# Optimization experiments

Measured on AMD Instinct MI355X. Metric: run time of the kernel, lower is better.

The kernel has to match this reference:

```python
import jax, jax.numpy as jnp
import numpy as np

N_NODES = 100000
N_EDGES = 1600000
IN_DIM, H1, H2, OUT_DIM = 128, 64, 32, 16


def setup_inputs() -> dict:
    key = jax.random.key(0)
    ks = jax.random.split(key, 9)
    x = jax.random.normal(ks[0], (N_NODES, IN_DIM), dtype=jnp.float32)
    edge_index = jax.random.randint(ks[1], (2, N_EDGES), 0, N_NODES, dtype=jnp.int64)
    # nn.Linear-style params (out_feats, in_feats) + bias
    def lin(k, o, i):
        bound = 1.0 / np.sqrt(i)
        kw, kb = jax.random.split(k)
        W = jax.random.uniform(kw, (o, i), jnp.float32, -bound, bound)
        b = jax.random.uniform(kb, (o,), jnp.float32, -bound, bound)
        return W, b
    W1, b1 = lin(ks[2], H1, IN_DIM)
    W2, b2 = lin(ks[3], H2, H1)
    Wf, bf = lin(ks[4], OUT_DIM, H2)
    return {"x": x, "edge_index": edge_index, "W1": W1, "b1": b1,
            "W2": W2, "b2": b2, "Wf": Wf, "bf": bf}


def reference(x, edge_index, W1, b1, W2, b2, Wf, bf):
    # Original: adj = to_dense_adj(edge_index); graph built from adj.T; DGL
    # copy_src+sum then gives new_h[src] = sum over dst of h[dst], i.e. A @ h
    # with A[src, dst]. No activation between layers (unused in forward),
    # dropout inactive at inference.
    N = x.shape[0]
    src, dst = edge_index[0], edge_index[1]

    def aggregate(h):  # sum of out-neighbor features: [N, d]
        return jax.ops.segment_sum(h[dst], src, num_segments=N)

    h = aggregate(x) @ W1.T + b1          # [N, 64]
    h = aggregate(h) @ W2.T + b2          # [N, 32]
    pooled = jnp.max(h, axis=0)           # [32] global max pool over nodes
    return pooled @ Wf.T + bf             # [16]
```

## Files before the change

kernel.cpp:

```cpp
#include <hip/hip_runtime.h>

#define N_NODES 100000
#define N_EDGES 1600000
#define IN_DIM 128
#define H1_DIM 64
#define H2_DIM 32
#define OUT_DIM 16

#define NPB 128
#define KB 782
#define OFFW (KB + 1)
#define NCH 256
#define CH_E (N_EDGES / NCH)
#define CAP2 3072
#define NBIN1 64
#define NBIN2 (NCH - NBIN1)
#define NGB 782

typedef __attribute__((ext_vector_type(8))) short short8;
typedef __attribute__((ext_vector_type(4))) float f32x4;

__device__ inline unsigned short f2b(float v) {
    unsigned u = __float_as_uint(v);
    u += 0x7FFF + ((u >> 16) & 1);
    return (unsigned short)(u >> 16);
}
__device__ inline short f2bs(float v) { return (short)f2b(v); }
__device__ inline unsigned f32_to_key(float v) {
    unsigned u = __float_as_uint(v);
    return (v >= 0.f) ? (u | 0x80000000u) : ~u;
}
__device__ __forceinline__ void acc8(float* a, uint4 v) {
    a[0] += __uint_as_float(v.x << 16);
    a[1] += __uint_as_float(v.x & 0xFFFF0000u);
    a[2] += __uint_as_float(v.y << 16);
    a[3] += __uint_as_float(v.y & 0xFFFF0000u);
    a[4] += __uint_as_float(v.z << 16);
    a[5] += __uint_as_float(v.z & 0xFFFF0000u);
    a[6] += __uint_as_float(v.w << 16);
    a[7] += __uint_as_float(v.w & 0xFFFF0000u);
}

__device__ __forceinline__ void bin_chunk(const int* __restrict__ src,
                                          const int* __restrict__ dst,
                                          unsigned* __restrict__ off,
                                          unsigned* __restrict__ grec, int c) {
    __shared__ int hist[1024];
    __shared__ int part[512];
    __shared__ int cur[1024];
    int t = threadIdx.x;
    int e0 = c * CH_E;
    hist[t] = 0; hist[t + 512] = 0;
    __syncthreads();
    for (int e = t; e < CH_E; e += 512) atomicAdd(&hist[src[e0 + e] >> 7], 1);
    __syncthreads();
    int h0 = hist[2 * t], h1 = hist[2 * t + 1];
    int tot = h0 + h1;
    part[t] = tot;
    __syncthreads();
    for (int o = 1; o < 512; o <<= 1) {
        int a = (t >= o) ? part[t - o] : 0;
        __syncthreads();
        part[t] += a;
        __syncthreads();
    }
    int gb = part[t] - tot;
    int o0 = gb, o1 = gb + h0;
    int b2i = 2 * t;
    cur[b2i] = o0; cur[b2i + 1] = o1;
    if (b2i + 0 < KB) off[(size_t)c * OFFW + b2i + 0] = o0;
    if (b2i + 1 < KB) off[(size_t)c * OFFW + b2i + 1] = o1;
    if (t == 0) off[(size_t)c * OFFW + KB] = CH_E;
    __syncthreads();
    for (int e = t; e < CH_E; e += 512) {
        int s = src[e0 + e];
        int d = dst[e0 + e];
        int p = atomicAdd(&cur[s >> 7], 1);
        grec[(size_t)e0 + p] = ((unsigned)(s & 127) << 17) | (unsigned)d;
    }
}

__global__ __launch_bounds__(512) void k1_kernel(const int* __restrict__ src,
                                                 const int* __restrict__ dst,
                                                 unsigned* __restrict__ off,
                                                 unsigned* __restrict__ grec,
                                                 const float* __restrict__ W1,
                                                 const float* __restrict__ b1,
                                                 const float* __restrict__ W2,
                                                 unsigned short* __restrict__ Wcb,
                                                 float* __restrict__ cvb) {
    if (blockIdx.x < NBIN1) {
        bin_chunk(src, dst, off, grec, blockIdx.x);
        return;
    }
    int t = threadIdx.x;
    for (int idx = t; idx < H2_DIM * IN_DIM; idx += 512) {
        int j = idx >> 7, f = idx & 127;
        float acc = 0.f;
        for (int k = 0; k < H1_DIM; ++k)
            acc += W2[j * H1_DIM + k] * W1[k * IN_DIM + f];
        Wcb[idx] = f2b(acc);
    }
    if (t < H2_DIM) {
        float s = 0.f;
        for (int k = 0; k < H1_DIM; ++k) s += W2[t * H1_DIM + k] * b1[k];
        cvb[t] = s;
    }
}

__global__ __launch_bounds__(512) void k2_kernel(const int* __restrict__ src,
                                                 const int* __restrict__ dst,
                                                 unsigned* __restrict__ off,
                                                 unsigned* __restrict__ grec,
                                                 const float* __restrict__ x,
                                                 const unsigned short* __restrict__ Wcb,
                                                 unsigned short* __restrict__ yb) {
    if (blockIdx.x < NBIN2) {
        bin_chunk(src, dst, off, grec, NBIN1 + blockIdx.x);
        return;
    }
    int gb = blockIdx.x - NBIN2;
    int t = threadIdx.x;
    int w = t >> 6, l = t & 63;
    int row = l & 15, kg = l >> 4;
    int base = gb * 128 + w * 16;
    int node = base + row;
    int nclamp = (node < N_NODES) ? node : (N_NODES - 1);
    const float* xp = x + (size_t)nclamp * IN_DIM + kg * 8;
    const unsigned short* b0p = Wcb + (size_t)row * IN_DIM + kg * 8;
    const unsigned short* b1p = Wcb + (size_t)(16 + row) * IN_DIM + kg * 8;
    f32x4 acc0 = {0.f, 0.f, 0.f, 0.f}, acc1 = {0.f, 0.f, 0.f, 0.f};
#pragma unroll
    for (int kk = 0; kk < 4; ++kk) {
        float4 xa = *(const float4*)(xp + kk * 32);
        float4 xb = *(const float4*)(xp + kk * 32 + 4);
        short8 a;
        a[0] = f2bs(xa.x); a[1] = f2bs(xa.y); a[2] = f2bs(xa.z); a[3] = f2bs(xa.w);
        a[4] = f2bs(xb.x); a[5] = f2bs(xb.y); a[6] = f2bs(xb.z); a[7] = f2bs(xb.w);
        short8 b0 = *(const short8*)(b0p + kk * 32);
        short8 b1 = *(const short8*)(b1p + kk * 32);
        acc0 = __builtin_amdgcn_mfma_f32_16x16x32_bf16(a, b0, acc0, 0, 0, 0);
        acc1 = __builtin_amdgcn_mfma_f32_16x16x32_bf16(a, b1, acc1, 0, 0, 0);
    }
#pragma unroll
    for (int r = 0; r < 4; ++r) {
        int n2 = base + kg * 4 + r;
        if (n2 < N_NODES) {
            yb[(size_t)n2 * H2_DIM + row]      = f2b(acc0[r]);
            yb[(size_t)n2 * H2_DIM + 16 + row] = f2b(acc1[r]);
        }
    }
}

__global__ __launch_bounds__(512) void agg1_kernel(const unsigned short* __restrict__ in,
                                                   const unsigned* __restrict__ off,
                                                   const unsigned* __restrict__ grec,
                                                   unsigned* __restrict__ grec2,
                                                   unsigned* __restrict__ noff,
                                                   unsigned short* __restrict__ z1b) {
    __shared__ int pos[NCH + 1], sst[NCH];
    __shared__ int shist[NPB], scur2[NPB];
    __shared__ int sscan[NPB + 1];
    __shared__ unsigned rbuf[CAP2];
    __shared__ unsigned sbuf[CAP2];
    __shared__ int s_cnt;
    int t = threadIdx.x;
    int b = blockIdx.x;
    int gid = t >> 4;
    int L = t & 15;
    int chunk = L & 3, subset = L >> 2;

    int mylen = 0;
    if (t < NCH) {
        unsigned o0 = off[(size_t)t * OFFW + b];
        unsigned o1 = off[(size_t)t * OFFW + b + 1];
        sst[t] = (int)o0;
        mylen = (int)(o1 - o0);
        pos[t] = mylen;
    }
    __syncthreads();
    for (int o = 1; o < NCH; o <<= 1) {
        int a = (t < NCH && t >= o) ? pos[t - o] : 0;
        __syncthreads();
        if (t < NCH) pos[t] += a;
        __syncthreads();
    }
    if (t < NCH) pos[t] -= mylen;
    if (t == NCH - 1) {
        pos[NCH] = pos[t] + mylen;
        s_cnt = min(pos[t] + mylen, CAP2);
    }
    __syncthreads();
    int cnt = s_cnt;
    for (int i = t; i < cnt; i += 512) {
        int lo = 0, hi = NCH;
#pragma unroll
        for (int s = 0; s < 8; ++s) {
            int mid = (lo + hi) >> 1;
            if (pos[mid] <= i) lo = mid; else hi = mid;
        }
        rbuf[i] = grec[(size_t)lo * CH_E + sst[lo] + (i - pos[lo])];
    }
    if (t < NPB) shist[t] = 0;
    __syncthreads();
    for (int i = t; i < cnt; i += 512) atomicAdd(&shist[rbuf[i] >> 17], 1);
    __syncthreads();
    if (t < NPB) scur2[t] = shist[t];
    __syncthreads();
    for (int o = 1; o < NPB; o <<= 1) {
        int a = (t < NPB && t >= o) ? scur2[t - o] : 0;
        __syncthreads();
        if (t < NPB) scur2[t] += a;
        __syncthreads();
    }
    if (t < NPB) sscan[t] = scur2[t] - shist[t];
    if (t == NPB - 1) sscan[NPB] = scur2[t];
    __syncthreads();
    if (t < NPB) scur2[t] = sscan[t];
    __syncthreads();
    for (int i = t; i < cnt; i += 512) {
        unsigned r = rbuf[i];
        int p = atomicAdd(&scur2[r >> 17], 1);
        if (p < CAP2) sbuf[p] = r;
    }
    __syncthreads();
    for (int i = t; i < cnt; i += 512) grec2[(size_t)b * CAP2 + i] = sbuf[i];
    if (t < NPB + 1) noff[(size_t)b * (NPB + 1) + t] = (unsigned)sscan[t];
    __syncthreads();

    for (int sl = gid; sl < NPB; sl += 32) {
        int r0 = sscan[sl], r1 = sscan[sl + 1];
        float a[8] = {0.f, 0.f, 0.f, 0.f, 0.f, 0.f, 0.f, 0.f};
        float aa[8] = {0.f, 0.f, 0.f, 0.f, 0.f, 0.f, 0.f, 0.f};
        for (int e = r0; e < r1; e += 8) {
            int eA = e + subset, eB = e + 4 + subset;
            if (eA < r1) {
                unsigned rc = sbuf[eA];
                uint4 v = *(const uint4*)(in + (size_t)(rc & 0x1FFFFu) * H2_DIM + chunk * 8);
                acc8(a, v);
            }
            if (eB < r1) {
                unsigned rc = sbuf[eB];
                uint4 v = *(const uint4*)(in + (size_t)(rc & 0x1FFFFu) * H2_DIM + chunk * 8);
                acc8(aa, v);
            }
        }
#pragma unroll
        for (int j = 0; j < 8; ++j) {
            float s = a[j] + aa[j];
            s += __shfl_xor(s, 4);
            s += __shfl_xor(s, 8);
            a[j] = s;
        }
        int node = b * NPB + sl;
        if (node < N_NODES && subset == 0) {
            uint4 o;
            o.x = (unsigned)f2b(a[0]) | ((unsigned)f2b(a[1]) << 16);
            o.y = (unsigned)f2b(a[2]) | ((unsigned)f2b(a[3]) << 16);
            o.z = (unsigned)f2b(a[4]) | ((unsigned)f2b(a[5]) << 16);
            o.w = (unsigned)f2b(a[6]) | ((unsigned)f2b(a[7]) << 16);
            *(uint4*)(z1b + (size_t)node * H2_DIM + chunk * 8) = o;
        }
    }
}

__global__ __launch_bounds__(1024) void agg2_kernel(const unsigned short* __restrict__ in,
                                                    const unsigned* __restrict__ grec2,
                                                    const unsigned* __restrict__ noff,
                                                    const float* __restrict__ cvb,
                                                    const float* __restrict__ b2,
                                                    unsigned* __restrict__ pk) {
    __shared__ float smq[64][4][8];
    int t = threadIdx.x;
    int b = blockIdx.x;
    int gid = t >> 4;
    int L = t & 15;
    int chunk = L & 3, subset = L >> 2;

    const unsigned* rp = grec2 + (size_t)b * CAP2;
    const unsigned* np = noff + (size_t)b * (NPB + 1);

    float m[8];
#pragma unroll
    for (int j = 0; j < 8; ++j) m[j] = -3.402823466e+38f;

    for (int sl = gid; sl < NPB; sl += 64) {
        int r0 = (int)np[sl], r1 = (int)np[sl + 1];
        float a[8] = {0.f, 0.f, 0.f, 0.f, 0.f, 0.f, 0.f, 0.f};
        float aa[8] = {0.f, 0.f, 0.f, 0.f, 0.f, 0.f, 0.f, 0.f};
        for (int e = r0; e < r1; e += 8) {
            int eA = e + subset, eB = e + 4 + subset;
            if (eA < r1) {
                unsigned rc = rp[eA];
                uint4 v = *(const uint4*)(in + (size_t)(rc & 0x1FFFFu) * H2_DIM + chunk * 8);
                acc8(a, v);
            }
            if (eB < r1) {
                unsigned rc = rp[eB];
                uint4 v = *(const uint4*)(in + (size_t)(rc & 0x1FFFFu) * H2_DIM + chunk * 8);
                acc8(aa, v);
            }
        }
#pragma unroll
        for (int j = 0; j < 8; ++j) {
            float s = a[j] + aa[j];
            s += __shfl_xor(s, 4);
            s += __shfl_xor(s, 8);
            a[j] = s;
        }
        int node = b * NPB + sl;
        if (node < N_NODES) {
            float dg = (float)(r1 - r0);
#pragma unroll
            for (int j = 0; j < 8; ++j)
                m[j] = fmaxf(m[j], a[j] + dg * cvb[chunk * 8 + j] + b2[chunk * 8 + j]);
        }
    }
    if (subset == 0) {
#pragma unroll
        for (int j = 0; j < 8; ++j) smq[gid][chunk][j] = m[j];
    }
    __syncthreads();
    if (t < 32) {
        int c = t >> 3, j = t & 7;
        float mm = smq[0][c][j];
#pragma unroll
        for (int k = 1; k < 64; ++k) mm = fmaxf(mm, smq[k][c][j]);
        atomicMax(&pk[t], f32_to_key(mm));
    }
}

__global__ void final_kernel(const unsigned* __restrict__ pk,
                             const float* __restrict__ Wf,
                             const float* __restrict__ bfv,
                             float* __restrict__ out) {
    __shared__ float pooled[H2_DIM];
    int t = threadIdx.x;
    if (t < H2_DIM) {
        unsigned k = pk[t];
        unsigned u = (k & 0x80000000u) ? (k & 0x7FFFFFFFu) : ~k;
        pooled[t] = __uint_as_float(u);
    }
    __syncthreads();
    if (t < OUT_DIM) {
        float acc = bfv[t];
        for (int j = 0; j < H2_DIM; ++j)
            acc += Wf[t * H2_DIM + j] * pooled[j];
        out[t] = acc;
    }
}

extern "C" void kernel_launch(void* const* d_in, const int* in_sizes, int n_in,
                              void* d_out, int out_size, void* d_ws, size_t ws_size,
                              hipStream_t stream) {
    const float* x  = (const float*)d_in[0];
    const int*   ei = (const int*)d_in[1];
    const float* W1 = (const float*)d_in[2];
    const float* b1 = (const float*)d_in[3];
    const float* W2 = (const float*)d_in[4];
    const float* b2 = (const float*)d_in[5];
    const float* Wf = (const float*)d_in[6];
    const float* bf = (const float*)d_in[7];
    float* out = (float*)d_out;

    const int* src = ei;
    const int* dst = ei + N_EDGES;

    unsigned short* yb  = (unsigned short*)d_ws;
    unsigned short* z1b = yb + (size_t)N_NODES * H2_DIM;
    unsigned short* Wcb = z1b + (size_t)N_NODES * H2_DIM;
    float* cvb      = (float*)(Wcb + H2_DIM * IN_DIM);
    unsigned* pk    = (unsigned*)(cvb + H2_DIM);
    unsigned* off   = pk + H2_DIM;
    unsigned* grec  = off + (size_t)NCH * OFFW;
    unsigned* grec2 = grec + N_EDGES;
    unsigned* noff  = grec2 + (size_t)KB * CAP2;

    hipMemsetAsync(pk, 0, H2_DIM * sizeof(unsigned), stream);

    k1_kernel<<<NBIN1 + 1, 512, 0, stream>>>(src, dst, off, grec, W1, b1, W2, Wcb, cvb);
    k2_kernel<<<NBIN2 + NGB, 512, 0, stream>>>(src, dst, off, grec, x, Wcb, yb);

    agg1_kernel<<<KB, 512, 0, stream>>>(yb, off, grec, grec2, noff, z1b);
    agg2_kernel<<<KB, 1024, 0, stream>>>(z1b, grec2, noff, cvb, b2, pk);

    final_kernel<<<1, 64, 0, stream>>>(pk, Wf, bf, out);
}
```

Measured before the change: 111.4 us.

## Use wavefront shuffle scans, transpose offset table, fold pool-init memset into k1

Replaces the shared-memory Hillis-Steele prefix scans in bin_chunk and agg1 with 64-lane shuffle scans plus a small per-wave sum combine, which removes most __syncthreads barriers. The per-chunk offset table is stored transposed, so each agg1 block reads its 256 chunk offsets contiguously instead of with a 783-element stride. The separate memset of the max-pool keys is moved into k1, dropping one stream operation. This adds some scattered writes in the binning blocks and relies on the existing kernel order to initialise pk before agg2 uses it.

```diff
diff --git a/kernel.cpp b/kernel.cpp
--- a/kernel.cpp
+++ b/kernel.cpp
@@ -9,7 +9,6 @@
 
 #define NPB 128
 #define KB 782
-#define OFFW (KB + 1)
 #define NCH 256
 #define CH_E (N_EDGES / NCH)
 #define CAP2 3072
@@ -43,11 +42,11 @@
 
 __device__ __forceinline__ void bin_chunk(const int* __restrict__ src,
                                           const int* __restrict__ dst,
-                                          unsigned* __restrict__ off,
+                                          unsigned* __restrict__ offT,
                                           unsigned* __restrict__ grec, int c) {
     __shared__ int hist[1024];
-    __shared__ int part[512];
     __shared__ int cur[1024];
+    __shared__ int bws[8];
     int t = threadIdx.x;
     int e0 = c * CH_E;
     hist[t] = 0; hist[t + 512] = 0;
@@ -56,21 +55,23 @@
     __syncthreads();
     int h0 = hist[2 * t], h1 = hist[2 * t + 1];
     int tot = h0 + h1;
-    part[t] = tot;
-    __syncthreads();
-    for (int o = 1; o < 512; o <<= 1) {
-        int a = (t >= o) ? part[t - o] : 0;
-        __syncthreads();
-        part[t] += a;
-        __syncthreads();
-    }
-    int gb = part[t] - tot;
+    int lane = t & 63, wv = t >> 6;
+    int sc = tot;
+    for (int o = 1; o < 64; o <<= 1) {
+        int n = __shfl_up(sc, o);
+        if (lane >= o) sc += n;
+    }
+    if (lane == 63) bws[wv] = sc;
+    __syncthreads();
+    int base = 0;
+    for (int k = 0; k < wv; ++k) base += bws[k];
+    int gb = base + sc - tot;
     int o0 = gb, o1 = gb + h0;
     int b2i = 2 * t;
     cur[b2i] = o0; cur[b2i + 1] = o1;
-    if (b2i + 0 < KB) off[(size_t)c * OFFW + b2i + 0] = o0;
-    if (b2i + 1 < KB) off[(size_t)c * OFFW + b2i + 1] = o1;
-    if (t == 0) off[(size_t)c * OFFW + KB] = CH_E;
+    if (b2i + 0 < KB) offT[(size_t)(b2i + 0) * NCH + c] = o0;
+    if (b2i + 1 < KB) offT[(size_t)(b2i + 1) * NCH + c] = o1;
+    if (t == 0) offT[(size_t)KB * NCH + c] = CH_E;
     __syncthreads();
     for (int e = t; e < CH_E; e += 512) {
         int s = src[e0 + e];
@@ -82,15 +83,16 @@
 
 __global__ __launch_bounds__(512) void k1_kernel(const int* __restrict__ src,
                                                  const int* __restrict__ dst,
-                                                 unsigned* __restrict__ off,
+                                                 unsigned* __restrict__ offT,
                                                  unsigned* __restrict__ grec,
                                                  const float* __restrict__ W1,
                                                  const float* __restrict__ b1,
                                                  const float* __restrict__ W2,
                                                  unsigned short* __restrict__ Wcb,
-                                                 float* __restrict__ cvb) {
+                                                 float* __restrict__ cvb,
+                                                 unsigned* __restrict__ pk) {
     if (blockIdx.x < NBIN1) {
-        bin_chunk(src, dst, off, grec, blockIdx.x);
+        bin_chunk(src, dst, offT, grec, blockIdx.x);
         return;
     }
     int t = threadIdx.x;
@@ -105,18 +107,19 @@
         float s = 0.f;
         for (int k = 0; k < H1_DIM; ++k) s += W2[t * H1_DIM + k] * b1[k];
         cvb[t] = s;
+        pk[t] = 0u;
     }
 }
 
 __global__ __launch_bounds__(512) void k2_kernel(const int* __restrict__ src,
                                                  const int* __restrict__ dst,
-                                                 unsigned* __restrict__ off,
+                                                 unsigned* __restrict__ offT,
                                                  unsigned* __restrict__ grec,
                                                  const float* __restrict__ x,
                                                  const unsigned short* __restrict__ Wcb,
                                                  unsigned short* __restrict__ yb) {
     if (blockIdx.x < NBIN2) {
-        bin_chunk(src, dst, off, grec, NBIN1 + blockIdx.x);
+        bin_chunk(src, dst, offT, grec, NBIN1 + blockIdx.x);
         return;
     }
     int gb = blockIdx.x - NBIN2;
@@ -153,7 +156,7 @@
 }
 
 __global__ __launch_bounds__(512) void agg1_kernel(const unsigned short* __restrict__ in,
-                                                   const unsigned* __restrict__ off,
+                                                   const unsigned* __restrict__ offT,
                                                    const unsigned* __restrict__ grec,
                                                    unsigned* __restrict__ grec2,
                                                    unsigned* __restrict__ noff,
@@ -161,6 +164,7 @@
     __shared__ int pos[NCH + 1], sst[NCH];
     __shared__ int shist[NPB], scur2[NPB];
     __shared__ int sscan[NPB + 1];
+    __shared__ int wsum[8];
     __shared__ unsigned rbuf[CAP2];
     __shared__ unsigned sbuf[CAP2];
     __shared__ int s_cnt;
@@ -169,27 +173,32 @@
     int gid = t >> 4;
     int L = t & 15;
     int chunk = L & 3, subset = L >> 2;
-
-    int mylen = 0;
+    int lane = t & 63, wv = t >> 6;
+
+    int mylen = 0, sc = 0;
     if (t < NCH) {
-        unsigned o0 = off[(size_t)t * OFFW + b];
-        unsigned o1 = off[(size_t)t * OFFW + b + 1];
+        unsigned o0 = offT[(size_t)b * NCH + t];
+        unsigned o1 = offT[(size_t)(b + 1) * NCH + t];
         sst[t] = (int)o0;
         mylen = (int)(o1 - o0);
-        pos[t] = mylen;
-    }
-    __syncthreads();
-    for (int o = 1; o < NCH; o <<= 1) {
-        int a = (t < NCH && t >= o) ? pos[t - o] : 0;
-        __syncthreads();
-        if (t < NCH) pos[t] += a;
-        __syncthreads();
-    }
-    if (t < NCH) pos[t] -= mylen;
-    if (t == NCH - 1) {
-        pos[NCH] = pos[t] + mylen;
-        s_cnt = min(pos[t] + mylen, CAP2);
-    }
+        sc = mylen;
+        for (int o = 1; o < 64; o <<= 1) {
+            int n = __shfl_up(sc, o);
+            if (lane >= o) sc += n;
+        }
+        if (lane == 63) wsum[wv] = sc;
+    }
+    __syncthreads();
+    if (t < NCH) {
+        int base = 0;
+        for (int k = 0; k < wv; ++k) base += wsum[k];
+        pos[t] = base + sc - mylen;
+        if (t == NCH - 1) {
+            pos[NCH] = base + sc;
+            s_cnt = min(base + sc, CAP2);
+        }
+    }
+    if (t < NPB) shist[t] = 0;
     __syncthreads();
     int cnt = s_cnt;
     for (int i = t; i < cnt; i += 512) {
@@ -201,22 +210,27 @@
         }
         rbuf[i] = grec[(size_t)lo * CH_E + sst[lo] + (i - pos[lo])];
     }
-    if (t < NPB) shist[t] = 0;
     __syncthreads();
     for (int i = t; i < cnt; i += 512) atomicAdd(&shist[rbuf[i] >> 17], 1);
     __syncthreads();
-    if (t < NPB) scur2[t] = shist[t];
-    __syncthreads();
-    for (int o = 1; o < NPB; o <<= 1) {
-        int a = (t < NPB && t >= o) ? scur2[t - o] : 0;
-        __syncthreads();
-        if (t < NPB) scur2[t] += a;
-        __syncthreads();
-    }
-    if (t < NPB) sscan[t] = scur2[t] - shist[t];
-    if (t == NPB - 1) sscan[NPB] = scur2[t];
-    __syncthreads();
-    if (t < NPB) scur2[t] = sscan[t];
+    int h = 0, sc2 = 0;
+    if (t < NPB) {
+        h = shist[t];
+        sc2 = h;
+        for (int o = 1; o < 64; o <<= 1) {
+            int n = __shfl_up(sc2, o);
+            if (lane >= o) sc2 += n;
+        }
+        if (lane == 63) wsum[4 + wv] = sc2;
+    }
+    __syncthreads();
+    if (t < NPB) {
+        int base = (wv == 1) ? wsum[4] : 0;
+        int ex = base + sc2 - h;
+        sscan[t] = ex;
+        scur2[t] = ex;
+        if (t == NPB - 1) sscan[NPB] = base + sc2;
+    }
     __syncthreads();
     for (int i = t; i < cnt; i += 512) {
         unsigned r = rbuf[i];
@@ -226,7 +240,6 @@
     __syncthreads();
     for (int i = t; i < cnt; i += 512) grec2[(size_t)b * CAP2 + i] = sbuf[i];
     if (t < NPB + 1) noff[(size_t)b * (NPB + 1) + t] = (unsigned)sscan[t];
-    __syncthreads();
 
     for (int sl = gid; sl < NPB; sl += 32) {
         int r0 = sscan[sl], r1 = sscan[sl + 1];
@@ -371,17 +384,16 @@
     unsigned short* Wcb = z1b + (size_t)N_NODES * H2_DIM;
     float* cvb      = (float*)(Wcb + H2_DIM * IN_DIM);
     unsigned* pk    = (unsigned*)(cvb + H2_DIM);
-    unsigned* off   = pk + H2_DIM;
-    unsigned* grec  = off + (size_t)NCH * OFFW;
+    unsigned* offT  = pk + H2_DIM;
+    unsigned* grec  = offT + (size_t)(KB + 1) * NCH;
     unsigned* grec2 = grec + N_EDGES;
     unsigned* noff  = grec2 + (size_t)KB * CAP2;
 
-    hipMemsetAsync(pk, 0, H2_DIM * sizeof(unsigned), stream);
-
-    k1_kernel<<<NBIN1 + 1, 512, 0, stream>>>(src, dst, off, grec, W1, b1, W2, Wcb, cvb);
-    k2_kernel<<<NBIN2 + NGB, 512, 0, stream>>>(src, dst, off, grec, x, Wcb, yb);
-
-    agg1_kernel<<<KB, 512, 0, stream>>>(yb, off, grec, grec2, noff, z1b);
+    k1_kernel<<<NBIN1 + 1, 512, 0, stream>>>(src, dst, offT, grec, W1, b1, W2,
+                                             Wcb, cvb, pk);
+    k2_kernel<<<NBIN2 + NGB, 512, 0, stream>>>(src, dst, offT, grec, x, Wcb, yb);
+
+    agg1_kernel<<<KB, 512, 0, stream>>>(yb, offT, grec, grec2, noff, z1b);
     agg2_kernel<<<KB, 1024, 0, stream>>>(z1b, grec2, noff, cvb, b2, pk);
 
     final_kernel<<<1, 64, 0, stream>>>(pk, Wf, bf, out);
```

New measurement: 105.5 us. 5.3% less time.
